# Optimization experiments

Measured on AMD Instinct MI355X. Metric: run time of the kernel, lower is better.

## Reference

```python
import jax, jax.numpy as jnp
import numpy as np

B, T, D, N = 16, 1024, 1024, 8


def setup_inputs() -> dict:
    key = jax.random.key(0)
    k1, k2, k3, k4 = jax.random.split(key, 4)
    s = 1.0 / np.sqrt(D)
    return {
        "x": jax.random.normal(k1, (B, T, D), dtype=jnp.float32),
        "W_h": jax.random.normal(k2, (D, D), dtype=jnp.float32) * (0.9 * s),
        "W_x": jax.random.normal(k3, (D, D), dtype=jnp.float32) * s,
        "b_h": jnp.zeros((D,), dtype=jnp.float32),
        "W_write": jax.random.normal(k4, (D, D), dtype=jnp.float32) * s,
    }


def reference(x, W_h, W_x, b_h, W_write):
    Bs, Ts, Ds = x.shape
    scale = 1.0 / Ds ** 0.5
    x_proj = jnp.einsum('btd,ed->bte', x, W_x)  # x @ W_x.T
    h_tape0 = jnp.zeros((Bs, N, Ds), dtype=x.dtype)
    h_work0 = jnp.zeros((Bs, Ds), dtype=x.dtype)

    def step(carry, x_t):
        h_tape, h_work = carry
        read_scores = jnp.einsum('bd,bnd->bn', h_work, h_tape) * scale
        read_attn = jax.nn.softmax(read_scores, axis=-1)
        read_val = jnp.einsum('bn,bnd->bd', read_attn, h_tape)
        Rh = h_work @ W_h.T
        h_work_new = jnp.tanh(x_t + Rh + read_val + b_h)
        write_val = h_work_new @ W_write.T
        write_scores = jnp.einsum('bd,bnd->bn', write_val, h_tape) * scale
        write_attn = jax.nn.softmax(write_scores, axis=-1)
        wa = write_attn[..., None]  # [B,N,1]
        h_tape_new = h_tape * (1.0 - wa) + write_val[:, None, :] * wa
        return (h_tape_new, h_work_new), h_work_new

    (h_tape_final, _), h_work_all = jax.lax.scan(
        step, (h_tape0, h_work0), jnp.swapaxes(x_proj, 0, 1))
    h_work_all = jnp.swapaxes(h_work_all, 0, 1)  # [B,T,D]
    return h_work_all, h_tape_final, h_work_all[:, -1, :]
```

## Files before the change

### kernel.cpp

```cpp
#include <hip/hip_runtime.h>
#include <math.h>

typedef __bf16 bf16x8 __attribute__((ext_vector_type(8)));
typedef float f32x4 __attribute__((ext_vector_type(4)));

namespace {

constexpr int kB = 16;
constexpr int kT = 1024;
constexpr int kD = 1024;
constexpr int kN = 8;
constexpr float kScale = 0.03125f;

constexpr unsigned long long kSent = ~0ull;
constexpr unsigned kSentW = 0xFFFFFFFFu;
constexpr int kHS = 3 * kB * kD;
constexpr int kRW = 2 * kB * kD;

__device__ inline unsigned short f2bf(float f) {
  unsigned u = __float_as_uint(f);
  u += 0x7FFFu + ((u >> 16) & 1u);
  return (unsigned short)(u >> 16);
}
__device__ inline float bf2f(unsigned short b) {
  return __uint_as_float(((unsigned)b) << 16);
}

__device__ inline float fast_tanh(float x) {
  const float ax = fabsf(x);
  const float t = __expf(-2.f * ax);
  const float r = (1.f - t) / (1.f + t);
  return copysignf(r, x);
}

__device__ inline void atst8(void* p, unsigned long long v) {
  __hip_atomic_store((unsigned long long*)p, v, __ATOMIC_RELAXED,
                     __HIP_MEMORY_SCOPE_AGENT);
}
__device__ inline unsigned long long atld8(const void* p) {
  return __hip_atomic_load((unsigned long long*)p, __ATOMIC_RELAXED,
                           __HIP_MEMORY_SCOPE_AGENT);
}
__device__ inline void atstf(float* p, float v) {
  __hip_atomic_store(p, v, __ATOMIC_RELAXED, __HIP_MEMORY_SCOPE_AGENT);
}
__device__ inline void atstu(unsigned* p, unsigned v) {
  __hip_atomic_store(p, v, __ATOMIC_RELAXED, __HIP_MEMORY_SCOPE_AGENT);
}
__device__ inline unsigned atldu(const unsigned* p) {
  return __hip_atomic_load((unsigned*)p, __ATOMIC_RELAXED,
                           __HIP_MEMORY_SCOPE_AGENT);
}

union U16 { unsigned long long ll[2]; unsigned wrd[4]; bf16x8 bv; float4 f4; };

__global__ __launch_bounds__(256)
void xproj_kernel(const float* __restrict__ X, const float* __restrict__ Wx,
                  float* __restrict__ C) {
  __shared__ float Xs[16][132];
  __shared__ float Ws[16][132];
  const int tid = threadIdx.x;
  const int n0 = blockIdx.x * 128;
  const int m0 = blockIdx.y * 128;
  const int tx = tid & 15;
  const int ty = tid >> 4;
  const int lr = tid >> 2;
  const int lc = (tid & 3) * 4;

  float acc[8][8];
#pragma unroll
  for (int i = 0; i < 8; ++i)
#pragma unroll
    for (int j = 0; j < 8; ++j) acc[i][j] = 0.f;

  for (int k0 = 0; k0 < kD; k0 += 16) {
    const float4 xa = *(const float4*)&X[(size_t)(m0 + lr) * kD + k0 + lc];
    const float4 xb = *(const float4*)&X[(size_t)(m0 + lr + 64) * kD + k0 + lc];
    const float4 wa = *(const float4*)&Wx[(size_t)(n0 + lr) * kD + k0 + lc];
    const float4 wb = *(const float4*)&Wx[(size_t)(n0 + lr + 64) * kD + k0 + lc];
    __syncthreads();
    Xs[lc + 0][lr] = xa.x; Xs[lc + 1][lr] = xa.y; Xs[lc + 2][lr] = xa.z; Xs[lc + 3][lr] = xa.w;
    Xs[lc + 0][lr + 64] = xb.x; Xs[lc + 1][lr + 64] = xb.y; Xs[lc + 2][lr + 64] = xb.z; Xs[lc + 3][lr + 64] = xb.w;
    Ws[lc + 0][lr] = wa.x; Ws[lc + 1][lr] = wa.y; Ws[lc + 2][lr] = wa.z; Ws[lc + 3][lr] = wa.w;
    Ws[lc + 0][lr + 64] = wb.x; Ws[lc + 1][lr + 64] = wb.y; Ws[lc + 2][lr + 64] = wb.z; Ws[lc + 3][lr + 64] = wb.w;
    __syncthreads();
#pragma unroll
    for (int k = 0; k < 16; ++k) {
      float a[8], b[8];
      *(float4*)&a[0] = *(const float4*)&Xs[k][ty * 8];
      *(float4*)&a[4] = *(const float4*)&Xs[k][ty * 8 + 4];
      *(float4*)&b[0] = *(const float4*)&Ws[k][tx * 8];
      *(float4*)&b[4] = *(const float4*)&Ws[k][tx * 8 + 4];
#pragma unroll
      for (int i = 0; i < 8; ++i)
#pragma unroll
        for (int j = 0; j < 8; ++j) acc[i][j] += a[i] * b[j];
    }
  }
#pragma unroll
  for (int i = 0; i < 8; ++i) {
    float4 v0 = make_float4(acc[i][0], acc[i][1], acc[i][2], acc[i][3]);
    float4 v1 = make_float4(acc[i][4], acc[i][5], acc[i][6], acc[i][7]);
    float* p = &C[(size_t)(m0 + ty * 8 + i) * kD + n0 + tx * 8];
    *(float4*)p = v0;
    *(float4*)(p + 4) = v1;
  }
}

__device__ inline void store_split(unsigned short* hs, int b, int d4, float4 h) {
  union { unsigned short u[4]; unsigned long long ll; } c2, c1, c0;
  float hv[4] = {h.x, h.y, h.z, h.w};
#pragma unroll
  for (int e = 0; e < 4; ++e) {
    unsigned short x = f2bf(hv[e]);
    float r = hv[e] - bf2f(x);
    unsigned short y = f2bf(r);
    float r2 = r - bf2f(y);
    unsigned short z = f2bf(r2);
    c2.u[e] = x; c1.u[e] = y; c0.u[e] = z;
  }
  const int w = d4 >> 8;
  const int j = (d4 >> 5) & 7;
  const int q = (d4 >> 3) & 3;
  const int hf = (d4 >> 2) & 1;
  const int off = ((w * 8 + j) << 9) + (hf << 8) + ((q * 16 + b) << 2);
  atst8(&hs[0 * 16384 + off], c2.ll);
  atst8(&hs[1 * 16384 + off], c1.ll);
  atst8(&hs[2 * 16384 + off], c0.ll);
}

__global__ __launch_bounds__(256, 1)
void scan_kernel(const float* __restrict__ Wh, const float* __restrict__ Ww,
                 const float* __restrict__ bh,
                 float* __restrict__ hall,
                 unsigned short* __restrict__ hsplit,
                 float* __restrict__ rw,
                 unsigned* __restrict__ hmark,
                 float* __restrict__ out_tape,
                 float* __restrict__ out_h) {
  const int g = blockIdx.x;
  const int tid = threadIdx.x;
  const int w = tid >> 6;
  const int ln = tid & 63;
  const int bat = ln & 15;
  const int q = ln >> 4;
  const bool tapeb = (g < kB);
  const int col0 = (g & 31) * 32;
  const int matw = g >> 5;

  __shared__ f32x4 Cred[2][4][2][64];
  __shared__ float red2[4][20];

  bf16x8 wf[3][2][8];
  {
    const float* Wsrc = matw ? Ww : Wh;
#pragma unroll
    for (int ct = 0; ct < 2; ++ct)
#pragma unroll
      for (int j = 0; j < 8; ++j) {
        const float* src = &Wsrc[(size_t)(col0 + ct * 16 + bat) * kD + (w * 8 + j) * 32 + q * 8];
        float v[8];
        *(float4*)&v[0] = *(const float4*)src;
        *(float4*)&v[4] = *(const float4*)(src + 4);
        union { unsigned short u[8]; bf16x8 b; } e2, e1, e0;
#pragma unroll
        for (int e = 0; e < 8; ++e) {
          unsigned short a = f2bf(v[e]);
          float r = v[e] - bf2f(a);
          unsigned short b2 = f2bf(r);
          float r2 = r - bf2f(b2);
          unsigned short c = f2bf(r2);
          e2.u[e] = a; e1.u[e] = b2; e0.u[e] = c;
        }
        wf[0][ct][j] = e2.b;
        wf[1][ct][j] = e1.b;
        wf[2][ct][j] = e0.b;
      }
  }

  float4 hprev = make_float4(0.f, 0.f, 0.f, 0.f);
  float4 bh4 = make_float4(0.f, 0.f, 0.f, 0.f);
  float4 tpr[kN];
#pragma unroll
  for (int n = 0; n < kN; ++n) tpr[n] = make_float4(0.f, 0.f, 0.f, 0.f);
  const int d4 = tid * 4;
  if (tapeb) {
    const size_t x0 = (size_t)g * kT * kD + d4;
    float4 xp0 = *(const float4*)&hall[x0];
    hprev.x = tanhf(xp0.x); hprev.y = tanhf(xp0.y);
    hprev.z = tanhf(xp0.z); hprev.w = tanhf(xp0.w);
    *(float4*)&hall[x0] = hprev;
    store_split(hsplit, g, d4, hprev);
    asm volatile("s_waitcnt vmcnt(0)" ::: "memory");
    if (ln == 0) atstu(&hmark[(w * 16 + g) * 16], 1u);
    bh4 = *(const float4*)&bh[d4];
  }

  for (int t = 0; t < kT; ++t) {
    const int p = t & 1;
    const unsigned short* hb = hsplit + p * kHS;

    float4 xp4 = make_float4(0.f, 0.f, 0.f, 0.f);
    if (tapeb && t < kT - 1)
      xp4 = *(const float4*)&hall[((size_t)g * kT + (t + 1)) * kD + d4];

    {
      const unsigned need = (unsigned)(t + 1);
      const unsigned* mk = &hmark[(w * 16 + bat) * 16];
      for (;;) {
        unsigned v = 0;
        if (q == 0) v = atldu(mk);
        v = __shfl(v, bat);
        if (v >= need) break;
        __builtin_amdgcn_s_sleep(1);
      }
      asm volatile("" ::: "memory");
    }
    U16 uf[3][8];
    const unsigned short* hw0 = hb + (w << 12) + (ln << 2);
    for (;;) {
      int bad = 0;
#pragma unroll
      for (int j = 0; j < 8; ++j) {
        const unsigned short* p0 = hw0 + (j << 9);
#pragma unroll
        for (int part = 0; part < 3; ++part) {
          uf[part][j].ll[0] = atld8(p0 + part * 16384);
          uf[part][j].ll[1] = atld8(p0 + part * 16384 + 256);
        }
      }
#pragma unroll
      for (int j = 0; j < 8; ++j)
#pragma unroll
        for (int part = 0; part < 3; ++part)
          bad |= (uf[part][j].ll[0] == kSent) | (uf[part][j].ll[1] == kSent);
      if (!bad) break;
      __builtin_amdgcn_s_sleep(1);
    }
    asm volatile("" ::: "memory");

    f32x4 zf = {0.f, 0.f, 0.f, 0.f};
    f32x4 acc[2][2] = {{zf, zf}, {zf, zf}};
#pragma unroll
    for (int j = 0; j < 8; ++j) {
      const int s = j & 1;
#pragma unroll
      for (int ct = 0; ct < 2; ++ct) {
        f32x4 a = acc[ct][s];
        a = __builtin_amdgcn_mfma_f32_16x16x32_bf16(uf[0][j].bv, wf[0][ct][j], a, 0, 0, 0);
        a = __builtin_amdgcn_mfma_f32_16x16x32_bf16(uf[0][j].bv, wf[1][ct][j], a, 0, 0, 0);
        a = __builtin_amdgcn_mfma_f32_16x16x32_bf16(uf[1][j].bv, wf[0][ct][j], a, 0, 0, 0);
        a = __builtin_amdgcn_mfma_f32_16x16x32_bf16(uf[0][j].bv, wf[2][ct][j], a, 0, 0, 0);
        a = __builtin_amdgcn_mfma_f32_16x16x32_bf16(uf[2][j].bv, wf[0][ct][j], a, 0, 0, 0);
        a = __builtin_amdgcn_mfma_f32_16x16x32_bf16(uf[1][j].bv, wf[1][ct][j], a, 0, 0, 0);
        acc[ct][s] = a;
      }
    }
    Cred[p][w][0][ln] = acc[0][0] + acc[0][1];
    Cred[p][w][1][ln] = acc[1][0] + acc[1][1];
    __syncthreads();
    if (tid < 128) {
      const int ct = tid >> 6, l2 = tid & 63;
      f32x4 sv = Cred[p][0][ct][l2] + Cred[p][1][ct][l2] +
                 Cred[p][2][ct][l2] + Cred[p][3][ct][l2];
      float* dst = rw + p * kRW + matw * (kB * kD);
      const int col = col0 + ct * 16 + (l2 & 15);
      const int m0 = (l2 >> 4) * 4;
#pragma unroll
      for (int r = 0; r < 4; ++r) atstf(&dst[(size_t)(m0 + r) * kD + col], sv[r]);
    }

    if (!tapeb) continue;

    const int b = g;
    float* rwp = rw + p * kRW;
    float* pr = &rwp[b * kD + d4];
    float* pw = &rwp[kB * kD + b * kD + d4];

    {
      float ph[kN];
#pragma unroll
      for (int n = 0; n < kN; ++n)
        ph[n] = hprev.x * tpr[n].x + hprev.y * tpr[n].y +
                hprev.z * tpr[n].z + hprev.w * tpr[n].w;
#pragma unroll
      for (int off = 32; off > 0; off >>= 1)
#pragma unroll
        for (int n = 0; n < kN; ++n) ph[n] += __shfl_xor(ph[n], off);
      if (ln == 0)
#pragma unroll
        for (int n = 0; n < kN; ++n) red2[w][8 + n] = ph[n];
    }

    float4 rh4, wv4;
    for (;;) {
      U16 ur, uw;
      ur.ll[0] = atld8(pr); ur.ll[1] = atld8(pr + 2);
      uw.ll[0] = atld8(pw); uw.ll[1] = atld8(pw + 2);
      int bad = 0;
#pragma unroll
      for (int k2 = 0; k2 < 4; ++k2)
        bad |= (ur.wrd[k2] == kSentW) | (uw.wrd[k2] == kSentW);
      if (!bad) { rh4 = ur.f4; wv4 = uw.f4; break; }
      __builtin_amdgcn_s_sleep(1);
    }
    asm volatile("" ::: "memory");
    atst8(pr, kSent); atst8(pr + 2, kSent);
    atst8(pw, kSent); atst8(pw + 2, kSent);

    {
      float pv[9];
#pragma unroll
      for (int n = 0; n < kN; ++n)
        pv[n] = wv4.x * tpr[n].x + wv4.y * tpr[n].y +
                wv4.z * tpr[n].z + wv4.w * tpr[n].w;
      pv[8] = hprev.x * wv4.x + hprev.y * wv4.y + hprev.z * wv4.z + hprev.w * wv4.w;
#pragma unroll
      for (int off = 32; off > 0; off >>= 1)
#pragma unroll
        for (int n = 0; n < 9; ++n) pv[n] += __shfl_xor(pv[n], off);
      if (ln == 0) {
#pragma unroll
        for (int n = 0; n < kN; ++n) red2[w][n] = pv[n];
        red2[w][16] = pv[8];
      }
    }
    __syncthreads();

    {
      unsigned short* hp0 = hsplit + p * kHS;
      const int off = (((d4 >> 8) * 8 + ((d4 >> 5) & 7)) << 9) +
                      (((d4 >> 2) & 1) << 8) + ((((d4 >> 3) & 3) * 16 + b) << 2);
      atst8(&hp0[0 * 16384 + off], kSent);
      atst8(&hp0[1 * 16384 + off], kSent);
      atst8(&hp0[2 * 16384 + off], kSent);
    }

    float s_h[kN], s_hwv;
    float wa[kN];
    {
      float mx = -1e30f;
#pragma unroll
      for (int n = 0; n < kN; ++n) {
        const float sc = kScale * (red2[0][n] + red2[1][n] + red2[2][n] + red2[3][n]);
        wa[n] = sc;
        mx = fmaxf(mx, sc);
        s_h[n] = red2[0][8 + n] + red2[1][8 + n] + red2[2][8 + n] + red2[3][8 + n];
      }
      s_hwv = red2[0][16] + red2[1][16] + red2[2][16] + red2[3][16];
      float ssum = 0.f;
#pragma unroll
      for (int n = 0; n < kN; ++n) { wa[n] = __expf(wa[n] - mx); ssum += wa[n]; }
      const float inv = 1.f / ssum;
#pragma unroll
      for (int n = 0; n < kN; ++n) wa[n] *= inv;
    }

#pragma unroll
    for (int n = 0; n < kN; ++n) {
      const float wn = wa[n], om = 1.f - wn;
      tpr[n].x = tpr[n].x * om + wv4.x * wn;
      tpr[n].y = tpr[n].y * om + wv4.y * wn;
      tpr[n].z = tpr[n].z * om + wv4.z * wn;
      tpr[n].w = tpr[n].w * om + wv4.w * wn;
    }

    if (t == kT - 1) {
#pragma unroll
      for (int n = 0; n < kN; ++n)
        *(float4*)&out_tape[((size_t)b * kN + n) * kD + d4] = tpr[n];
      *(float4*)&out_h[b * kD + d4] = hprev;
      continue;
    }

    float ra[kN];
    {
      float mx = -1e30f;
#pragma unroll
      for (int n = 0; n < kN; ++n) {
        const float sc = kScale * (s_h[n] * (1.f - wa[n]) + s_hwv * wa[n]);
        ra[n] = sc;
        mx = fmaxf(mx, sc);
      }
      float ssum = 0.f;
#pragma unroll
      for (int n = 0; n < kN; ++n) { ra[n] = __expf(ra[n] - mx); ssum += ra[n]; }
      const float inv = 1.f / ssum;
#pragma unroll
      for (int n = 0; n < kN; ++n) ra[n] *= inv;
    }

    float4 rv = make_float4(0.f, 0.f, 0.f, 0.f);
#pragma unroll
    for (int n = 0; n < kN; ++n) {
      rv.x += ra[n] * tpr[n].x; rv.y += ra[n] * tpr[n].y;
      rv.z += ra[n] * tpr[n].z; rv.w += ra[n] * tpr[n].w;
    }

    float4 hn;
    hn.x = fast_tanh(xp4.x + rh4.x + rv.x + bh4.x);
    hn.y = fast_tanh(xp4.y + rh4.y + rv.y + bh4.y);
    hn.z = fast_tanh(xp4.z + rh4.z + rv.z + bh4.z);
    hn.w = fast_tanh(xp4.w + rh4.w + rv.w + bh4.w);

    asm volatile("s_waitcnt vmcnt(0)" ::: "memory");
    store_split(hsplit + (p ^ 1) * kHS, b, d4, hn);
    if (ln == 0) atstu(&hmark[(w * 16 + b) * 16], (unsigned)(t + 2));
    *(float4*)&hall[((size_t)b * kT + (t + 1)) * kD + d4] = hn;
    hprev = hn;
  }
}

}

extern "C" void kernel_launch(void* const* d_in, const int* in_sizes, int n_in,
                              void* d_out, int out_size, void* d_ws, size_t ws_size,
                              hipStream_t stream) {
  const float* x  = (const float*)d_in[0];
  const float* Wh = (const float*)d_in[1];
  const float* Wx = (const float*)d_in[2];
  const float* bh = (const float*)d_in[3];
  const float* Ww = (const float*)d_in[4];

  float* out = (float*)d_out;
  float* hall = out;
  float* out_tape = out + (size_t)kB * kT * kD;
  float* out_h = out_tape + (size_t)kB * kN * kD;

  unsigned* hmark = (unsigned*)d_ws;
  unsigned short* hsplit = (unsigned short*)((char*)d_ws + 4096);
  float* rw = (float*)((char*)d_ws + 4096 + 2 * kHS * (int)sizeof(unsigned short));

  hipMemsetAsync(d_ws, 0, 4096, stream);
  hipMemsetAsync((char*)d_ws + 4096, 0xFF,
                 2 * kHS * sizeof(unsigned short) + 2 * kRW * sizeof(float),
                 stream);

  xproj_kernel<<<dim3(kD / 128, (kB * kT) / 128), 256, 0, stream>>>(x, Wx, hall);

  scan_kernel<<<64, 256, 0, stream>>>(Wh, Ww, bh, hall, hsplit, rw, hmark,
                                      out_tape, out_h);
}
```

Measured before the change: 9.744 ms.

## Fuse input projection GEMM into scan kernel and overlap via sentinel polling

The separate x-projection GEMM launch is merged into the persistent scan kernel: 64 blocks run the recurrence while 1024 extra blocks compute x@W_x tiles ordered by time, writing results with atomic stores. The output buffer is pre-filled with a 0xFF sentinel, and the scan blocks spin on each x_proj value until it is no longer the sentinel. The intent is to hide the GEMM behind the sequential scan instead of running it first. The cost is an extra 64 MB memset, polling loads, and GEMM blocks competing with the scan blocks for CUs and memory bandwidth. Correctness also depends on the scan blocks being resident alongside the GEMM blocks.

```diff
diff --git a/kernel.cpp b/kernel.cpp
--- a/kernel.cpp
+++ b/kernel.cpp
@@ -53,59 +53,6 @@
 }
 
 union U16 { unsigned long long ll[2]; unsigned wrd[4]; bf16x8 bv; float4 f4; };
-
-__global__ __launch_bounds__(256)
-void xproj_kernel(const float* __restrict__ X, const float* __restrict__ Wx,
-                  float* __restrict__ C) {
-  __shared__ float Xs[16][132];
-  __shared__ float Ws[16][132];
-  const int tid = threadIdx.x;
-  const int n0 = blockIdx.x * 128;
-  const int m0 = blockIdx.y * 128;
-  const int tx = tid & 15;
-  const int ty = tid >> 4;
-  const int lr = tid >> 2;
-  const int lc = (tid & 3) * 4;
-
-  float acc[8][8];
-#pragma unroll
-  for (int i = 0; i < 8; ++i)
-#pragma unroll
-    for (int j = 0; j < 8; ++j) acc[i][j] = 0.f;
-
-  for (int k0 = 0; k0 < kD; k0 += 16) {
-    const float4 xa = *(const float4*)&X[(size_t)(m0 + lr) * kD + k0 + lc];
-    const float4 xb = *(const float4*)&X[(size_t)(m0 + lr + 64) * kD + k0 + lc];
-    const float4 wa = *(const float4*)&Wx[(size_t)(n0 + lr) * kD + k0 + lc];
-    const float4 wb = *(const float4*)&Wx[(size_t)(n0 + lr + 64) * kD + k0 + lc];
-    __syncthreads();
-    Xs[lc + 0][lr] = xa.x; Xs[lc + 1][lr] = xa.y; Xs[lc + 2][lr] = xa.z; Xs[lc + 3][lr] = xa.w;
-    Xs[lc + 0][lr + 64] = xb.x; Xs[lc + 1][lr + 64] = xb.y; Xs[lc + 2][lr + 64] = xb.z; Xs[lc + 3][lr + 64] = xb.w;
-    Ws[lc + 0][lr] = wa.x; Ws[lc + 1][lr] = wa.y; Ws[lc + 2][lr] = wa.z; Ws[lc + 3][lr] = wa.w;
-    Ws[lc + 0][lr + 64] = wb.x; Ws[lc + 1][lr + 64] = wb.y; Ws[lc + 2][lr + 64] = wb.z; Ws[lc + 3][lr + 64] = wb.w;
-    __syncthreads();
-#pragma unroll
-    for (int k = 0; k < 16; ++k) {
-      float a[8], b[8];
-      *(float4*)&a[0] = *(const float4*)&Xs[k][ty * 8];
-      *(float4*)&a[4] = *(const float4*)&Xs[k][ty * 8 + 4];
-      *(float4*)&b[0] = *(const float4*)&Ws[k][tx * 8];
-      *(float4*)&b[4] = *(const float4*)&Ws[k][tx * 8 + 4];
-#pragma unroll
-      for (int i = 0; i < 8; ++i)
-#pragma unroll
-        for (int j = 0; j < 8; ++j) acc[i][j] += a[i] * b[j];
-    }
-  }
-#pragma unroll
-  for (int i = 0; i < 8; ++i) {
-    float4 v0 = make_float4(acc[i][0], acc[i][1], acc[i][2], acc[i][3]);
-    float4 v1 = make_float4(acc[i][4], acc[i][5], acc[i][6], acc[i][7]);
-    float* p = &C[(size_t)(m0 + ty * 8 + i) * kD + n0 + tx * 8];
-    *(float4*)p = v0;
-    *(float4*)(p + 4) = v1;
-  }
-}
 
 __device__ inline void store_split(unsigned short* hs, int b, int d4, float4 h) {
   union { unsigned short u[4]; unsigned long long ll; } c2, c1, c0;
@@ -130,7 +77,8 @@
 }
 
 __global__ __launch_bounds__(256, 1)
-void scan_kernel(const float* __restrict__ Wh, const float* __restrict__ Ww,
+void scan_kernel(const float* __restrict__ X, const float* __restrict__ Wx,
+                 const float* __restrict__ Wh, const float* __restrict__ Ww,
                  const float* __restrict__ bh,
                  float* __restrict__ hall,
                  unsigned short* __restrict__ hsplit,
@@ -138,19 +86,79 @@
                  unsigned* __restrict__ hmark,
                  float* __restrict__ out_tape,
                  float* __restrict__ out_h) {
-  const int g = blockIdx.x;
+  __shared__ float Xs[16][132];
+  __shared__ float Ws[16][132];
+  __shared__ f32x4 Cred[2][4][2][64];
+  __shared__ float red2[4][20];
+
+  const int bid = blockIdx.x;
   const int tid = threadIdx.x;
+
+  if (bid >= 64) {
+    const int e = bid - 64;
+    const int t_blk = e >> 7;
+    const int b = (e >> 3) & 15;
+    const int nb = e & 7;
+    const int m0 = b * kT + t_blk * 128;
+    const int n0 = nb * 128;
+    const int tx = tid & 15;
+    const int ty = tid >> 4;
+    const int lr = tid >> 2;
+    const int lc = (tid & 3) * 4;
+
+    float acc[8][8];
+#pragma unroll
+    for (int i = 0; i < 8; ++i)
+#pragma unroll
+      for (int j = 0; j < 8; ++j) acc[i][j] = 0.f;
+
+    for (int k0 = 0; k0 < kD; k0 += 16) {
+      const float4 xa = *(const float4*)&X[(size_t)(m0 + lr) * kD + k0 + lc];
+      const float4 xb = *(const float4*)&X[(size_t)(m0 + lr + 64) * kD + k0 + lc];
+      const float4 wa = *(const float4*)&Wx[(size_t)(n0 + lr) * kD + k0 + lc];
+      const float4 wb = *(const float4*)&Wx[(size_t)(n0 + lr + 64) * kD + k0 + lc];
+      __syncthreads();
+      Xs[lc + 0][lr] = xa.x; Xs[lc + 1][lr] = xa.y; Xs[lc + 2][lr] = xa.z; Xs[lc + 3][lr] = xa.w;
+      Xs[lc + 0][lr + 64] = xb.x; Xs[lc + 1][lr + 64] = xb.y; Xs[lc + 2][lr + 64] = xb.z; Xs[lc + 3][lr + 64] = xb.w;
+      Ws[lc + 0][lr] = wa.x; Ws[lc + 1][lr] = wa.y; Ws[lc + 2][lr] = wa.z; Ws[lc + 3][lr] = wa.w;
+      Ws[lc + 0][lr + 64] = wb.x; Ws[lc + 1][lr + 64] = wb.y; Ws[lc + 2][lr + 64] = wb.z; Ws[lc + 3][lr + 64] = wb.w;
+      __syncthreads();
+#pragma unroll
+      for (int k = 0; k < 16; ++k) {
+        float a[8], bb[8];
+        *(float4*)&a[0] = *(const float4*)&Xs[k][ty * 8];
+        *(float4*)&a[4] = *(const float4*)&Xs[k][ty * 8 + 4];
+        *(float4*)&bb[0] = *(const float4*)&Ws[k][tx * 8];
+        *(float4*)&bb[4] = *(const float4*)&Ws[k][tx * 8 + 4];
+#pragma unroll
+        for (int i = 0; i < 8; ++i)
+#pragma unroll
+          for (int j = 0; j < 8; ++j) acc[i][j] += a[i] * bb[j];
+      }
+    }
+#pragma unroll
+    for (int i = 0; i < 8; ++i) {
+      union { float f[8]; unsigned long long ll[4]; } row;
+#pragma unroll
+      for (int j = 0; j < 8; ++j) row.f[j] = acc[i][j];
+      float* p = &hall[(size_t)(m0 + ty * 8 + i) * kD + n0 + tx * 8];
+      atst8(p + 0, row.ll[0]);
+      atst8(p + 2, row.ll[1]);
+      atst8(p + 4, row.ll[2]);
+      atst8(p + 6, row.ll[3]);
+    }
+    return;
+  }
+
+  const int g = bid;
   const int w = tid >> 6;
   const int ln = tid & 63;
   const int bat = ln & 15;
-  const int q = ln >> 4;
+  const int q = tid >> 4 & 3;
   const bool tapeb = (g < kB);
   const int col0 = (g & 31) * 32;
   const int matw = g >> 5;
 
-  __shared__ f32x4 Cred[2][4][2][64];
-  __shared__ float red2[4][20];
-
   bf16x8 wf[3][2][8];
   {
     const float* Wsrc = matw ? Ww : Wh;
@@ -158,7 +166,7 @@
     for (int ct = 0; ct < 2; ++ct)
 #pragma unroll
       for (int j = 0; j < 8; ++j) {
-        const float* src = &Wsrc[(size_t)(col0 + ct * 16 + bat) * kD + (w * 8 + j) * 32 + q * 8];
+        const float* src = &Wsrc[(size_t)(col0 + ct * 16 + bat) * kD + (w * 8 + j) * 32 + ((ln >> 4)) * 8];
         float v[8];
         *(float4*)&v[0] = *(const float4*)src;
         *(float4*)&v[4] = *(const float4*)(src + 4);
@@ -177,6 +185,7 @@
         wf[2][ct][j] = e0.b;
       }
   }
+  (void)q;
 
   float4 hprev = make_float4(0.f, 0.f, 0.f, 0.f);
   float4 bh4 = make_float4(0.f, 0.f, 0.f, 0.f);
@@ -185,11 +194,20 @@
   for (int n = 0; n < kN; ++n) tpr[n] = make_float4(0.f, 0.f, 0.f, 0.f);
   const int d4 = tid * 4;
   if (tapeb) {
-    const size_t x0 = (size_t)g * kT * kD + d4;
-    float4 xp0 = *(const float4*)&hall[x0];
-    hprev.x = tanhf(xp0.x); hprev.y = tanhf(xp0.y);
-    hprev.z = tanhf(xp0.z); hprev.w = tanhf(xp0.w);
-    *(float4*)&hall[x0] = hprev;
+    float* px0 = &hall[(size_t)g * kT * kD + d4];
+    U16 ux;
+    for (;;) {
+      ux.ll[0] = atld8(px0); ux.ll[1] = atld8(px0 + 2);
+      int bad = 0;
+#pragma unroll
+      for (int k2 = 0; k2 < 4; ++k2) bad |= (ux.wrd[k2] == kSentW);
+      if (!bad) break;
+      __builtin_amdgcn_s_sleep(1);
+    }
+    asm volatile("" ::: "memory");
+    hprev.x = tanhf(ux.f4.x); hprev.y = tanhf(ux.f4.y);
+    hprev.z = tanhf(ux.f4.z); hprev.w = tanhf(ux.f4.w);
+    *(float4*)px0 = hprev;
     store_split(hsplit, g, d4, hprev);
     asm volatile("s_waitcnt vmcnt(0)" ::: "memory");
     if (ln == 0) atstu(&hmark[(w * 16 + g) * 16], 1u);
@@ -200,16 +218,19 @@
     const int p = t & 1;
     const unsigned short* hb = hsplit + p * kHS;
 
-    float4 xp4 = make_float4(0.f, 0.f, 0.f, 0.f);
-    if (tapeb && t < kT - 1)
-      xp4 = *(const float4*)&hall[((size_t)g * kT + (t + 1)) * kD + d4];
+    U16 uxp;
+    float* px = nullptr;
+    if (tapeb && t < kT - 1) {
+      px = &hall[((size_t)g * kT + (t + 1)) * kD + d4];
+      uxp.ll[0] = atld8(px); uxp.ll[1] = atld8(px + 2);
+    }
 
     {
       const unsigned need = (unsigned)(t + 1);
       const unsigned* mk = &hmark[(w * 16 + bat) * 16];
       for (;;) {
         unsigned v = 0;
-        if (q == 0) v = atldu(mk);
+        if ((ln >> 4) == 0) v = atldu(mk);
         v = __shfl(v, bat);
         if (v >= need) break;
         __builtin_amdgcn_s_sleep(1);
@@ -397,6 +418,17 @@
       rv.z += ra[n] * tpr[n].z; rv.w += ra[n] * tpr[n].w;
     }
 
+    for (;;) {
+      int bad = 0;
+#pragma unroll
+      for (int k2 = 0; k2 < 4; ++k2) bad |= (uxp.wrd[k2] == kSentW);
+      if (!bad) break;
+      __builtin_amdgcn_s_sleep(1);
+      uxp.ll[0] = atld8(px); uxp.ll[1] = atld8(px + 2);
+    }
+    asm volatile("" ::: "memory");
+    const float4 xp4 = uxp.f4;
+
     float4 hn;
     hn.x = fast_tanh(xp4.x + rh4.x + rv.x + bh4.x);
     hn.y = fast_tanh(xp4.y + rh4.y + rv.y + bh4.y);
@@ -435,9 +467,9 @@
   hipMemsetAsync((char*)d_ws + 4096, 0xFF,
                  2 * kHS * sizeof(unsigned short) + 2 * kRW * sizeof(float),
                  stream);
-
-  xproj_kernel<<<dim3(kD / 128, (kB * kT) / 128), 256, 0, stream>>>(x, Wx, hall);
-
-  scan_kernel<<<64, 256, 0, stream>>>(Wh, Ww, bh, hall, hsplit, rw, hmark,
-                                      out_tape, out_h);
-}
+  hipMemsetAsync(hall, 0xFF, (size_t)kB * kT * kD * sizeof(float),
+                 stream);
+
+  scan_kernel<<<64 + 1024, 256, 0, stream>>>(x, Wx, Wh, Ww, bh, hall, hsplit,
+                                             rw, hmark, out_tape, out_h);
+}
```

Result: faster. 9.280 ms (-4.8%).
